# Kernel tuning notes

Measured on AMD Instinct MI355X. Metric: run time of the kernel, lower is better.

Reference implementation:

```python
import jax, jax.numpy as jnp
import numpy as np

EPS = 1e-07
GAMMA = 2.0
LAMBDA_DISCO = 1000.0


def _binary_entropy(target, output):
    x = jnp.clip(output, EPS, 1.0 - EPS)
    return -target * jnp.log(x) - (1.0 - target) * jnp.log(1.0 - x)


def _focal_bce(target, output, y_class, y_pred_class):
    yc = y_class[:, 0]
    ypc = y_pred_class[:, 0]
    y_pred = output[:, 0]
    bce = _binary_entropy(target, y_pred)
    m = jnp.mean(ypc)
    s = jnp.std(ypc)  # population std, matches tf.math.reduce_std
    norm = jnp.clip((ypc - m) / (2.0 * s) + 0.5, 0.0, 1.0)
    class_weight_factor = ((1.0 - yc) * norm) ** GAMMA
    norm_factor = jnp.sum(1.0 - yc) / jnp.sum(class_weight_factor)
    return class_weight_factor * bce * norm_factor


def _distance_corr(var_1, var_2, w, power):
    # pairwise |x_i - x_j| distance matrices [N, N]
    amat = jnp.abs(var_1[:, None] - var_1[None, :])
    bmat = jnp.abs(var_2[:, None] - var_2[None, :])
    amatavg = jnp.mean(amat * w, axis=1)
    bmatavg = jnp.mean(bmat * w, axis=1)
    # double centering (tile layout: minuend_1[i,j]=avg[j], minuend_2[i,j]=avg[i])
    Amat = amat - amatavg[None, :] - amatavg[:, None] + jnp.mean(amatavg * w)
    Bmat = bmat - bmatavg[None, :] - bmatavg[:, None] + jnp.mean(bmatavg * w)
    ABavg = jnp.abs(jnp.mean(Amat * Bmat * w, axis=1))
    AAavg = jnp.mean(Amat * Amat * w, axis=1)
    BBavg = jnp.mean(Bmat * Bmat * w, axis=1)
    mAB = jnp.mean(ABavg * w)
    mAA = jnp.mean(AAavg * w)
    mBB = jnp.mean(BBavg * w)
    if power == 1:
        dCorr = mAB / jnp.sqrt(jnp.abs(mAA * mBB) + 1e-12)
    elif power == 2:
        dCorr = mAB ** 2 / (jnp.abs(mAA * mBB) + 1e-12)
    else:
        dCorr = (mAB / jnp.sqrt(mAA * mBB) + 1e-12) ** power
    dCorr = jnp.where(jnp.isnan(dCorr), 0.0, dCorr)
    dCorr = jnp.where(dCorr < 0.0, 0.0, dCorr)
    return dCorr


def setup_inputs() -> dict:
    N = 4096
    key = jax.random.key(0)
    ks = jax.random.split(key, 6)
    target = jnp.round(jax.random.uniform(ks[0], (N,), dtype=jnp.float32))
    output = jax.random.uniform(ks[1], (N, 1), dtype=jnp.float32, minval=0.02, maxval=0.98)
    y_class = jnp.round(jax.random.uniform(ks[2], (N, 1), dtype=jnp.float32))
    y_pred_class = jax.random.uniform(ks[3], (N, 1), dtype=jnp.float32, minval=0.02, maxval=0.98)
    var_1 = jax.random.normal(ks[4], (N,), dtype=jnp.float32) * 20.0 + 100.0  # mass-like
    var_2 = jax.random.uniform(ks[5], (N,), dtype=jnp.float32)  # classifier-output-like
    normedweight = jnp.ones((N,), dtype=jnp.float32)  # sums to N as required
    return {"target": target, "output": output, "y_class": y_class,
            "y_pred_class": y_pred_class, "var_1": var_1, "var_2": var_2,
            "normedweight": normedweight, "power": 1}


def reference(target, output, y_class, y_pred_class, var_1, var_2, normedweight, power):
    focal = _focal_bce(target, output, y_class, y_pred_class)
    dcorr = _distance_corr(var_1, var_2, normedweight, power)
    return jnp.mean(focal) + LAMBDA_DISCO * dcorr
```

## Files before the change

### kernel.cpp

```cpp
#include <hip/hip_runtime.h>
#include <math.h>

#define N     4096
#define NBLK  256
#define RPB   16
#define FEPS  1e-7f


__device__ __forceinline__ double block_reduce(double v) {
    __shared__ double buf[4];
    int tid = threadIdx.x;
#pragma unroll
    for (int o = 32; o > 0; o >>= 1) v += __shfl_down(v, o, 64);
    __syncthreads();
    if ((tid & 63) == 0) buf[tid >> 6] = v;
    __syncthreads();
    return buf[0] + buf[1] + buf[2] + buf[3];
}

__global__ __launch_bounds__(256) void k1(
        const float* __restrict__ y_class,
        const float* __restrict__ y_pred_class,
        const float* __restrict__ v1,
        const float* __restrict__ v2,
        const float* __restrict__ w,
        double* __restrict__ pf,
        double* __restrict__ pg,
        float*  __restrict__ rowA,
        float*  __restrict__ rowB)
{
    __shared__ float s1[N], s2[N], sw[N];
    __shared__ float rsA[RPB], rsB[RPB];
    const int tid = threadIdx.x;
    const int b   = blockIdx.x;

    for (int t = tid * 4; t < N; t += 1024) {
        *(float4*)&s1[t] = *(const float4*)&v1[t];
        *(float4*)&s2[t] = *(const float4*)&v2[t];
        *(float4*)&sw[t] = *(const float4*)&w [t];
    }

    if (tid < 16) {
        int i = b * RPB + tid;
        float ypc = y_pred_class[i];
        float yc  = y_class[i];
        double sy  = (double)ypc;
        double sy2 = (double)ypc * (double)ypc;
        double syc = (double)yc;
#pragma unroll
        for (int o = 1; o < 16; o <<= 1) {
            sy  += __shfl_xor(sy,  o, 16);
            sy2 += __shfl_xor(sy2, o, 16);
            syc += __shfl_xor(syc, o, 16);
        }
        if (tid == 0) { pf[b] = sy; pf[NBLK + b] = sy2; pf[2 * NBLK + b] = syc; }
    }
    __syncthreads();

    const int lane = tid & 63;
    const int g    = tid >> 6;
    const int i0   = b * RPB + g * 4;
    float a0 = s1[i0+0], a1 = s1[i0+1], a2 = s1[i0+2], a3 = s1[i0+3];
    float e0 = s2[i0+0], e1 = s2[i0+1], e2 = s2[i0+2], e3 = s2[i0+3];
    float sa0=0.f,sa1=0.f,sa2=0.f,sa3=0.f, sb0=0.f,sb1=0.f,sb2=0.f,sb3=0.f;
#pragma unroll 4
    for (int k = 0; k < N / (64 * 4); ++k) {
        int j = 4 * lane + 256 * k;
        float4 x1 = *(const float4*)&s1[j];
        float4 x2 = *(const float4*)&s2[j];
        float4 xw = *(const float4*)&sw[j];
#define P1(c)                                      \
        sa0 = fmaf(fabsf(a0 - x1.c), xw.c, sa0);   \
        sa1 = fmaf(fabsf(a1 - x1.c), xw.c, sa1);   \
        sa2 = fmaf(fabsf(a2 - x1.c), xw.c, sa2);   \
        sa3 = fmaf(fabsf(a3 - x1.c), xw.c, sa3);   \
        sb0 = fmaf(fabsf(e0 - x2.c), xw.c, sb0);   \
        sb1 = fmaf(fabsf(e1 - x2.c), xw.c, sb1);   \
        sb2 = fmaf(fabsf(e2 - x2.c), xw.c, sb2);   \
        sb3 = fmaf(fabsf(e3 - x2.c), xw.c, sb3);
        P1(x) P1(y) P1(z) P1(w)
#undef P1
    }
#pragma unroll
    for (int o = 1; o < 64; o <<= 1) {
        sa0 += __shfl_xor(sa0, o, 64); sa1 += __shfl_xor(sa1, o, 64);
        sa2 += __shfl_xor(sa2, o, 64); sa3 += __shfl_xor(sa3, o, 64);
        sb0 += __shfl_xor(sb0, o, 64); sb1 += __shfl_xor(sb1, o, 64);
        sb2 += __shfl_xor(sb2, o, 64); sb3 += __shfl_xor(sb3, o, 64);
    }
    if (lane == 0) {
        rowA[i0+0]=sa0; rowA[i0+1]=sa1; rowA[i0+2]=sa2; rowA[i0+3]=sa3;
        rowB[i0+0]=sb0; rowB[i0+1]=sb1; rowB[i0+2]=sb2; rowB[i0+3]=sb3;
        rsA[g*4+0]=sa0; rsA[g*4+1]=sa1; rsA[g*4+2]=sa2; rsA[g*4+3]=sa3;
        rsB[g*4+0]=sb0; rsB[g*4+1]=sb1; rsB[g*4+2]=sb2; rsB[g*4+3]=sb3;
    }
    __syncthreads();
    if (tid == 0) {
        double ga = 0.0, gb = 0.0;
#pragma unroll
        for (int q = 0; q < RPB; ++q) {
            double wq = (double)sw[b * RPB + q];
            ga += (double)rsA[q] * wq;
            gb += (double)rsB[q] * wq;
        }
        pg[b] = ga; pg[NBLK + b] = gb;
    }
}

__global__ __launch_bounds__(256) void k2(
        const float* __restrict__ target,
        const float* __restrict__ output,
        const float* __restrict__ y_class,
        const float* __restrict__ y_pred_class,
        const float* __restrict__ v1,
        const float* __restrict__ v2,
        const float* __restrict__ w,
        const float* __restrict__ rowA,
        const float* __restrict__ rowB,
        const double* __restrict__ pf,
        const double* __restrict__ pg,
        const int*   __restrict__ power,
        unsigned int* __restrict__ cntB,
        double* __restrict__ pr,
        float*  __restrict__ out)
{
    __shared__ float s1[N], s2[N], sw[N], sav[N], sbv[N];
    __shared__ double rd[3][RPB];
    const int tid = threadIdx.x;
    const int b   = blockIdx.x;
    const float invN = 1.0f / (float)N;

    for (int t = tid * 4; t < N; t += 1024) {
        *(float4*)&s1[t] = *(const float4*)&v1[t];
        *(float4*)&s2[t] = *(const float4*)&v2[t];
        *(float4*)&sw[t] = *(const float4*)&w [t];
        float4 ra = *(const float4*)&rowA[t];
        float4 rb = *(const float4*)&rowB[t];
        ra.x *= invN; ra.y *= invN; ra.z *= invN; ra.w *= invN;
        rb.x *= invN; rb.y *= invN; rb.z *= invN; rb.w *= invN;
        *(float4*)&sav[t] = ra;
        *(float4*)&sbv[t] = rb;
    }
    __syncthreads();

    const double NN = (double)N * (double)N;
    float gA = (float)(block_reduce(pg[tid]) / NN);
    float gB = (float)(block_reduce(pg[NBLK + tid]) / NN);
    double t_ypc  = block_reduce(pf[tid]);
    double t_ypc2 = block_reduce(pf[NBLK + tid]);
    double fm   = t_ypc / (double)N;
    double fvar = t_ypc2 / (double)N - fm * fm;
    double fsd  = sqrt(fvar > 0.0 ? fvar : 0.0);
    float  m    = (float)fm;
    float  inv2s = (float)(1.0 / (2.0 * fsd));

    if (tid < 16) {
        int i = b * RPB + tid;
        float yc  = y_class[i];
        float ypc = y_pred_class[i];
        float nrm = (ypc - m) * inv2s + 0.5f;
        nrm = fminf(fmaxf(nrm, 0.0f), 1.0f);
        float c1  = (1.0f - yc) * nrm;
        float cwf = c1 * c1;
        float x = fminf(fmaxf(output[i], FEPS), 1.0f - FEPS);
        float t = target[i];
        float bce = -t * logf(x) - (1.0f - t) * logf(1.0f - x);
        double scwf  = (double)cwf;
        double scwfb = (double)cwf * (double)bce;
#pragma unroll
        for (int o = 1; o < 16; o <<= 1) {
            scwf  += __shfl_xor(scwf,  o, 16);
            scwfb += __shfl_xor(scwfb, o, 16);
        }
        if (tid == 0) { pr[3 * NBLK + b] = scwf; pr[4 * NBLK + b] = scwfb; }
    }

    const int lane = tid & 63;
    const int g    = tid >> 6;
    const int i0   = b * RPB + g * 4;
    float a0 = s1[i0+0], a1 = s1[i0+1], a2 = s1[i0+2], a3 = s1[i0+3];
    float e0 = s2[i0+0], e1 = s2[i0+1], e2 = s2[i0+2], e3 = s2[i0+3];
    float cA0 = sav[i0+0] - gA, cA1 = sav[i0+1] - gA,
          cA2 = sav[i0+2] - gA, cA3 = sav[i0+3] - gA;
    float cB0 = sbv[i0+0] - gB, cB1 = sbv[i0+1] - gB,
          cB2 = sbv[i0+2] - gB, cB3 = sbv[i0+3] - gB;

    float ab0=0.f,ab1=0.f,ab2=0.f,ab3=0.f;
    float aa0=0.f,aa1=0.f,aa2=0.f,aa3=0.f;
    float bb0=0.f,bb1=0.f,bb2=0.f,bb3=0.f;
#pragma unroll 2
    for (int k = 0; k < N / (64 * 4); ++k) {
        int j = 4 * lane + 256 * k;
        float4 x1 = *(const float4*)&s1[j];
        float4 x2 = *(const float4*)&s2[j];
        float4 xw = *(const float4*)&sw[j];
        float4 xa = *(const float4*)&sav[j];
        float4 xb = *(const float4*)&sbv[j];
#define P2(c, r)                                                  \
        {                                                         \
            float Am = fabsf(a##r - x1.c) - xa.c - cA##r;         \
            float Bm = fabsf(e##r - x2.c) - xb.c - cB##r;         \
            float Aw = Am * xw.c;                                 \
            float Bw = Bm * xw.c;                                 \
            ab##r = fmaf(Aw, Bm, ab##r);                          \
            aa##r = fmaf(Aw, Am, aa##r);                          \
            bb##r = fmaf(Bw, Bm, bb##r);                          \
        }
#define P2ALL(c) P2(c,0) P2(c,1) P2(c,2) P2(c,3)
        P2ALL(x) P2ALL(y) P2ALL(z) P2ALL(w)
#undef P2ALL
#undef P2
    }
#pragma unroll
    for (int o = 1; o < 64; o <<= 1) {
        ab0 += __shfl_xor(ab0, o, 64); ab1 += __shfl_xor(ab1, o, 64);
        ab2 += __shfl_xor(ab2, o, 64); ab3 += __shfl_xor(ab3, o, 64);
        aa0 += __shfl_xor(aa0, o, 64); aa1 += __shfl_xor(aa1, o, 64);
        aa2 += __shfl_xor(aa2, o, 64); aa3 += __shfl_xor(aa3, o, 64);
        bb0 += __shfl_xor(bb0, o, 64); bb1 += __shfl_xor(bb1, o, 64);
        bb2 += __shfl_xor(bb2, o, 64); bb3 += __shfl_xor(bb3, o, 64);
    }
    if (lane == 0) {
        double w0 = (double)sw[i0+0], w1 = (double)sw[i0+1];
        double w2 = (double)sw[i0+2], w3 = (double)sw[i0+3];
        rd[0][g*4+0] = fabs((double)ab0) * w0; rd[0][g*4+1] = fabs((double)ab1) * w1;
        rd[0][g*4+2] = fabs((double)ab2) * w2; rd[0][g*4+3] = fabs((double)ab3) * w3;
        rd[1][g*4+0] = (double)aa0 * w0;       rd[1][g*4+1] = (double)aa1 * w1;
        rd[1][g*4+2] = (double)aa2 * w2;       rd[1][g*4+3] = (double)aa3 * w3;
        rd[2][g*4+0] = (double)bb0 * w0;       rd[2][g*4+1] = (double)bb1 * w1;
        rd[2][g*4+2] = (double)bb2 * w2;       rd[2][g*4+3] = (double)bb3 * w3;
    }
    __syncthreads();

    __shared__ int isLast;
    if (tid == 0) {
        double tab = 0.0, taa = 0.0, tbb = 0.0;
#pragma unroll
        for (int q = 0; q < RPB; ++q) { tab += rd[0][q]; taa += rd[1][q]; tbb += rd[2][q]; }
        pr[b] = tab; pr[NBLK + b] = taa; pr[2 * NBLK + b] = tbb;
        __threadfence();
        unsigned int old = atomicAdd(cntB, 1u);
        isLast = (old == NBLK - 1);
    }
    __syncthreads();
    if (!isLast) return;
    __threadfence();

    double tab   = block_reduce(pr[tid]);
    double taa   = block_reduce(pr[NBLK + tid]);
    double tbb   = block_reduce(pr[2 * NBLK + tid]);
    double tcwf  = block_reduce(pr[3 * NBLK + tid]);
    double tcwfb = block_reduce(pr[4 * NBLK + tid]);
    double t_yc  = block_reduce(pf[2 * NBLK + tid]);
    if (tid == 0) {
        double focal = tcwfb * (((double)N - t_yc) / tcwf) / (double)N;
        double mAB = tab / NN;
        double mAA = taa / NN;
        double mBB = tbb / NN;
        int p = power[0];
        double d;
        if (p == 1) {
            d = mAB / sqrt(fabs(mAA * mBB) + 1e-12);
        } else if (p == 2) {
            d = (mAB * mAB) / (fabs(mAA * mBB) + 1e-12);
        } else {
            d = pow(mAB / sqrt(mAA * mBB) + 1e-12, (double)p);
        }
        if (isnan(d)) d = 0.0;
        if (d < 0.0)  d = 0.0;
        out[0] = (float)(focal + 1000.0 * d);
    }
}

extern "C" void kernel_launch(void* const* d_in, const int* in_sizes, int n_in,
                              void* d_out, int out_size, void* d_ws, size_t ws_size,
                              hipStream_t stream) {
    const float* target       = (const float*)d_in[0];
    const float* output       = (const float*)d_in[1];
    const float* y_class      = (const float*)d_in[2];
    const float* y_pred_class = (const float*)d_in[3];
    const float* var_1        = (const float*)d_in[4];
    const float* var_2        = (const float*)d_in[5];
    const float* normedweight = (const float*)d_in[6];
    const int*   power        = (const int*)d_in[7];
    float* out = (float*)d_out;

    char*         ws   = (char*)d_ws;
    unsigned int* cntB = (unsigned int*)ws;
    double*       pf   = (double*)(ws + 64);
    double*       pg   = (double*)(ws + 64 + 6144);
    double*       pr   = (double*)(ws + 64 + 6144 + 4096);
    float*        rowA = (float*)(ws + 64 + 6144 + 4096 + 10240);
    float*        rowB = rowA + N;

    hipMemsetAsync(ws, 0, 4, stream);
    k1<<<NBLK, 256, 0, stream>>>(y_class, y_pred_class, var_1, var_2, normedweight,
                                 pf, pg, rowA, rowB);
    k2<<<NBLK, 256, 0, stream>>>(target, output, y_class, y_pred_class,
                                 var_1, var_2, normedweight, rowA, rowB,
                                 pf, pg, power, cntB, pr, out);
}
```

Before: 36.48 us.

## Split work across 512 blocks with half-column tiles and drop memset launch

Raises the grid from 256 to 512 blocks. In k1 each block now covers one half of the columns and writes partial row sums per half. In k2 each block handles 8 rows and loops over two half-size shared tiles, so shared memory per block is halved and occupancy should rise. The counter reset moves from a separate hipMemsetAsync into k1, which removes one launch. In exchange k2 stages its shared data twice, with extra syncs and extra global reads of the partial rows.

```diff
diff --git a/kernel.cpp b/kernel.cpp
--- a/kernel.cpp
+++ b/kernel.cpp
@@ -2,8 +2,8 @@
 #include <math.h>
 
 #define N     4096
-#define NBLK  256
-#define RPB   16
+#define HALF  2048
+#define NB    512
 #define FEPS  1e-7f
 
 
@@ -24,24 +24,30 @@
         const float* __restrict__ v1,
         const float* __restrict__ v2,
         const float* __restrict__ w,
+        unsigned int* __restrict__ cntB,
         double* __restrict__ pf,
         double* __restrict__ pg,
-        float*  __restrict__ rowA,
-        float*  __restrict__ rowB)
+        float*  __restrict__ rowA_p,
+        float*  __restrict__ rowB_p)
 {
-    __shared__ float s1[N], s2[N], sw[N];
-    __shared__ float rsA[RPB], rsB[RPB];
+    __shared__ float s1[HALF], s2[HALF], sw[HALF];
+    __shared__ float rsA[16], rsB[16];
     const int tid = threadIdx.x;
     const int b   = blockIdx.x;
-
-    for (int t = tid * 4; t < N; t += 1024) {
-        *(float4*)&s1[t] = *(const float4*)&v1[t];
-        *(float4*)&s2[t] = *(const float4*)&v2[t];
-        *(float4*)&sw[t] = *(const float4*)&w [t];
-    }
-
-    if (tid < 16) {
-        int i = b * RPB + tid;
+    const int rb  = b >> 1;
+    const int h   = b & 1;
+    const int j0  = h * HALF;
+
+    if (b == 0 && tid == 0) *cntB = 0;
+
+    for (int t = tid * 4; t < HALF; t += 1024) {
+        *(float4*)&s1[t] = *(const float4*)&v1[j0 + t];
+        *(float4*)&s2[t] = *(const float4*)&v2[j0 + t];
+        *(float4*)&sw[t] = *(const float4*)&w [j0 + t];
+    }
+
+    if (h == 0 && tid < 16) {
+        int i = rb * 16 + tid;
         float ypc = y_pred_class[i];
         float yc  = y_class[i];
         double sy  = (double)ypc;
@@ -53,18 +59,18 @@
             sy2 += __shfl_xor(sy2, o, 16);
             syc += __shfl_xor(syc, o, 16);
         }
-        if (tid == 0) { pf[b] = sy; pf[NBLK + b] = sy2; pf[2 * NBLK + b] = syc; }
+        if (tid == 0) { pf[rb] = sy; pf[256 + rb] = sy2; pf[512 + rb] = syc; }
     }
     __syncthreads();
 
     const int lane = tid & 63;
     const int g    = tid >> 6;
-    const int i0   = b * RPB + g * 4;
-    float a0 = s1[i0+0], a1 = s1[i0+1], a2 = s1[i0+2], a3 = s1[i0+3];
-    float e0 = s2[i0+0], e1 = s2[i0+1], e2 = s2[i0+2], e3 = s2[i0+3];
+    const int i0   = rb * 16 + g * 4;
+    float a0 = v1[i0+0], a1 = v1[i0+1], a2 = v1[i0+2], a3 = v1[i0+3];
+    float e0 = v2[i0+0], e1 = v2[i0+1], e2 = v2[i0+2], e3 = v2[i0+3];
     float sa0=0.f,sa1=0.f,sa2=0.f,sa3=0.f, sb0=0.f,sb1=0.f,sb2=0.f,sb3=0.f;
-#pragma unroll 4
-    for (int k = 0; k < N / (64 * 4); ++k) {
+#pragma unroll
+    for (int k = 0; k < HALF / (64 * 4); ++k) {
         int j = 4 * lane + 256 * k;
         float4 x1 = *(const float4*)&s1[j];
         float4 x2 = *(const float4*)&s2[j];
@@ -89,21 +95,24 @@
         sb2 += __shfl_xor(sb2, o, 64); sb3 += __shfl_xor(sb3, o, 64);
     }
     if (lane == 0) {
-        rowA[i0+0]=sa0; rowA[i0+1]=sa1; rowA[i0+2]=sa2; rowA[i0+3]=sa3;
-        rowB[i0+0]=sb0; rowB[i0+1]=sb1; rowB[i0+2]=sb2; rowB[i0+3]=sb3;
+        rowA_p[h*N + i0+0]=sa0; rowA_p[h*N + i0+1]=sa1;
+        rowA_p[h*N + i0+2]=sa2; rowA_p[h*N + i0+3]=sa3;
+        rowB_p[h*N + i0+0]=sb0; rowB_p[h*N + i0+1]=sb1;
+        rowB_p[h*N + i0+2]=sb2; rowB_p[h*N + i0+3]=sb3;
         rsA[g*4+0]=sa0; rsA[g*4+1]=sa1; rsA[g*4+2]=sa2; rsA[g*4+3]=sa3;
         rsB[g*4+0]=sb0; rsB[g*4+1]=sb1; rsB[g*4+2]=sb2; rsB[g*4+3]=sb3;
     }
     __syncthreads();
-    if (tid == 0) {
-        double ga = 0.0, gb = 0.0;
-#pragma unroll
-        for (int q = 0; q < RPB; ++q) {
-            double wq = (double)sw[b * RPB + q];
-            ga += (double)rsA[q] * wq;
-            gb += (double)rsB[q] * wq;
-        }
-        pg[b] = ga; pg[NBLK + b] = gb;
+    if (tid < 16) {
+        double wq = (double)w[rb * 16 + tid];
+        double da = (double)rsA[tid] * wq;
+        double db = (double)rsB[tid] * wq;
+#pragma unroll
+        for (int o = 1; o < 16; o <<= 1) {
+            da += __shfl_xor(da, o, 16);
+            db += __shfl_xor(db, o, 16);
+        }
+        if (tid == 0) { pg[b] = da; pg[NB + b] = db; }
     }
 }
 
@@ -115,8 +124,8 @@
         const float* __restrict__ v1,
         const float* __restrict__ v2,
         const float* __restrict__ w,
-        const float* __restrict__ rowA,
-        const float* __restrict__ rowB,
+        const float* __restrict__ rowA_p,
+        const float* __restrict__ rowB_p,
         const double* __restrict__ pf,
         const double* __restrict__ pg,
         const int*   __restrict__ power,
@@ -124,38 +133,25 @@
         double* __restrict__ pr,
         float*  __restrict__ out)
 {
-    __shared__ float s1[N], s2[N], sw[N], sav[N], sbv[N];
-    __shared__ double rd[3][RPB];
+    __shared__ float s1[HALF], s2[HALF], sw[HALF], sav[HALF], sbv[HALF];
+    __shared__ double rd[3][8];
     const int tid = threadIdx.x;
     const int b   = blockIdx.x;
     const float invN = 1.0f / (float)N;
-
-    for (int t = tid * 4; t < N; t += 1024) {
-        *(float4*)&s1[t] = *(const float4*)&v1[t];
-        *(float4*)&s2[t] = *(const float4*)&v2[t];
-        *(float4*)&sw[t] = *(const float4*)&w [t];
-        float4 ra = *(const float4*)&rowA[t];
-        float4 rb = *(const float4*)&rowB[t];
-        ra.x *= invN; ra.y *= invN; ra.z *= invN; ra.w *= invN;
-        rb.x *= invN; rb.y *= invN; rb.z *= invN; rb.w *= invN;
-        *(float4*)&sav[t] = ra;
-        *(float4*)&sbv[t] = rb;
-    }
-    __syncthreads();
-
     const double NN = (double)N * (double)N;
-    float gA = (float)(block_reduce(pg[tid]) / NN);
-    float gB = (float)(block_reduce(pg[NBLK + tid]) / NN);
+
+    float gA = (float)(block_reduce(pg[tid]      + pg[256 + tid]) / NN);
+    float gB = (float)(block_reduce(pg[NB + tid] + pg[NB + 256 + tid]) / NN);
     double t_ypc  = block_reduce(pf[tid]);
-    double t_ypc2 = block_reduce(pf[NBLK + tid]);
+    double t_ypc2 = block_reduce(pf[256 + tid]);
     double fm   = t_ypc / (double)N;
     double fvar = t_ypc2 / (double)N - fm * fm;
     double fsd  = sqrt(fvar > 0.0 ? fvar : 0.0);
-    float  m    = (float)fm;
+    float  m     = (float)fm;
     float  inv2s = (float)(1.0 / (2.0 * fsd));
 
-    if (tid < 16) {
-        int i = b * RPB + tid;
+    if (b < 256 && tid < 16) {
+        int i = b * 16 + tid;
         float yc  = y_class[i];
         float ypc = y_pred_class[i];
         float nrm = (ypc - m) * inv2s + 0.5f;
@@ -172,63 +168,75 @@
             scwf  += __shfl_xor(scwf,  o, 16);
             scwfb += __shfl_xor(scwfb, o, 16);
         }
-        if (tid == 0) { pr[3 * NBLK + b] = scwf; pr[4 * NBLK + b] = scwfb; }
+        if (tid == 0) { pr[3 * NB + b] = scwf; pr[3 * NB + 256 + b] = scwfb; }
     }
 
     const int lane = tid & 63;
     const int g    = tid >> 6;
-    const int i0   = b * RPB + g * 4;
-    float a0 = s1[i0+0], a1 = s1[i0+1], a2 = s1[i0+2], a3 = s1[i0+3];
-    float e0 = s2[i0+0], e1 = s2[i0+1], e2 = s2[i0+2], e3 = s2[i0+3];
-    float cA0 = sav[i0+0] - gA, cA1 = sav[i0+1] - gA,
-          cA2 = sav[i0+2] - gA, cA3 = sav[i0+3] - gA;
-    float cB0 = sbv[i0+0] - gB, cB1 = sbv[i0+1] - gB,
-          cB2 = sbv[i0+2] - gB, cB3 = sbv[i0+3] - gB;
-
-    float ab0=0.f,ab1=0.f,ab2=0.f,ab3=0.f;
-    float aa0=0.f,aa1=0.f,aa2=0.f,aa3=0.f;
-    float bb0=0.f,bb1=0.f,bb2=0.f,bb3=0.f;
-#pragma unroll 2
-    for (int k = 0; k < N / (64 * 4); ++k) {
-        int j = 4 * lane + 256 * k;
-        float4 x1 = *(const float4*)&s1[j];
-        float4 x2 = *(const float4*)&s2[j];
-        float4 xw = *(const float4*)&sw[j];
-        float4 xa = *(const float4*)&sav[j];
-        float4 xb = *(const float4*)&sbv[j];
+    const int i0   = b * 8 + g * 2;
+    float a0 = v1[i0+0], a1 = v1[i0+1];
+    float e0 = v2[i0+0], e1 = v2[i0+1];
+    float cA0 = (rowA_p[i0+0] + rowA_p[N+i0+0]) * invN - gA;
+    float cA1 = (rowA_p[i0+1] + rowA_p[N+i0+1]) * invN - gA;
+    float cB0 = (rowB_p[i0+0] + rowB_p[N+i0+0]) * invN - gB;
+    float cB1 = (rowB_p[i0+1] + rowB_p[N+i0+1]) * invN - gB;
+
+    float ab0=0.f,aa0=0.f,bb0=0.f, ab1=0.f,aa1=0.f,bb1=0.f;
+    for (int h = 0; h < 2; ++h) {
+        int j0 = h * HALF;
+        __syncthreads();
+        for (int t = tid * 4; t < HALF; t += 1024) {
+            *(float4*)&s1[t] = *(const float4*)&v1[j0 + t];
+            *(float4*)&s2[t] = *(const float4*)&v2[j0 + t];
+            *(float4*)&sw[t] = *(const float4*)&w [j0 + t];
+            float4 r0 = *(const float4*)&rowA_p[j0 + t];
+            float4 r1 = *(const float4*)&rowA_p[N + j0 + t];
+            float4 q0 = *(const float4*)&rowB_p[j0 + t];
+            float4 q1 = *(const float4*)&rowB_p[N + j0 + t];
+            float4 ra, rbv;
+            ra.x  = (r0.x + r1.x) * invN;  ra.y  = (r0.y + r1.y) * invN;
+            ra.z  = (r0.z + r1.z) * invN;  ra.w  = (r0.w + r1.w) * invN;
+            rbv.x = (q0.x + q1.x) * invN;  rbv.y = (q0.y + q1.y) * invN;
+            rbv.z = (q0.z + q1.z) * invN;  rbv.w = (q0.w + q1.w) * invN;
+            *(float4*)&sav[t] = ra;
+            *(float4*)&sbv[t] = rbv;
+        }
+        __syncthreads();
+#pragma unroll
+        for (int k = 0; k < HALF / (64 * 4); ++k) {
+            int j = 4 * lane + 256 * k;
+            float4 x1 = *(const float4*)&s1[j];
+            float4 x2 = *(const float4*)&s2[j];
+            float4 xw = *(const float4*)&sw[j];
+            float4 xa = *(const float4*)&sav[j];
+            float4 xb = *(const float4*)&sbv[j];
 #define P2(c, r)                                                  \
-        {                                                         \
-            float Am = fabsf(a##r - x1.c) - xa.c - cA##r;         \
-            float Bm = fabsf(e##r - x2.c) - xb.c - cB##r;         \
-            float Aw = Am * xw.c;                                 \
-            float Bw = Bm * xw.c;                                 \
-            ab##r = fmaf(Aw, Bm, ab##r);                          \
-            aa##r = fmaf(Aw, Am, aa##r);                          \
-            bb##r = fmaf(Bw, Bm, bb##r);                          \
-        }
-#define P2ALL(c) P2(c,0) P2(c,1) P2(c,2) P2(c,3)
-        P2ALL(x) P2ALL(y) P2ALL(z) P2ALL(w)
+            {                                                     \
+                float Am = fabsf(a##r - x1.c) - xa.c - cA##r;     \
+                float Bm = fabsf(e##r - x2.c) - xb.c - cB##r;     \
+                float Aw = Am * xw.c;                             \
+                float Bw = Bm * xw.c;                             \
+                ab##r = fmaf(Aw, Bm, ab##r);                      \
+                aa##r = fmaf(Aw, Am, aa##r);                      \
+                bb##r = fmaf(Bw, Bm, bb##r);                      \
+            }
+#define P2ALL(c) P2(c,0) P2(c,1)
+            P2ALL(x) P2ALL(y) P2ALL(z) P2ALL(w)
 #undef P2ALL
 #undef P2
+        }
     }
 #pragma unroll
     for (int o = 1; o < 64; o <<= 1) {
         ab0 += __shfl_xor(ab0, o, 64); ab1 += __shfl_xor(ab1, o, 64);
-        ab2 += __shfl_xor(ab2, o, 64); ab3 += __shfl_xor(ab3, o, 64);
         aa0 += __shfl_xor(aa0, o, 64); aa1 += __shfl_xor(aa1, o, 64);
-        aa2 += __shfl_xor(aa2, o, 64); aa3 += __shfl_xor(aa3, o, 64);
         bb0 += __shfl_xor(bb0, o, 64); bb1 += __shfl_xor(bb1, o, 64);
-        bb2 += __shfl_xor(bb2, o, 64); bb3 += __shfl_xor(bb3, o, 64);
     }
     if (lane == 0) {
-        double w0 = (double)sw[i0+0], w1 = (double)sw[i0+1];
-        double w2 = (double)sw[i0+2], w3 = (double)sw[i0+3];
-        rd[0][g*4+0] = fabs((double)ab0) * w0; rd[0][g*4+1] = fabs((double)ab1) * w1;
-        rd[0][g*4+2] = fabs((double)ab2) * w2; rd[0][g*4+3] = fabs((double)ab3) * w3;
-        rd[1][g*4+0] = (double)aa0 * w0;       rd[1][g*4+1] = (double)aa1 * w1;
-        rd[1][g*4+2] = (double)aa2 * w2;       rd[1][g*4+3] = (double)aa3 * w3;
-        rd[2][g*4+0] = (double)bb0 * w0;       rd[2][g*4+1] = (double)bb1 * w1;
-        rd[2][g*4+2] = (double)bb2 * w2;       rd[2][g*4+3] = (double)bb3 * w3;
+        double w0 = (double)w[i0+0], w1 = (double)w[i0+1];
+        rd[0][g*2+0] = fabs((double)ab0) * w0;  rd[0][g*2+1] = fabs((double)ab1) * w1;
+        rd[1][g*2+0] = (double)aa0 * w0;        rd[1][g*2+1] = (double)aa1 * w1;
+        rd[2][g*2+0] = (double)bb0 * w0;        rd[2][g*2+1] = (double)bb1 * w1;
     }
     __syncthreads();
 
@@ -236,22 +244,22 @@
     if (tid == 0) {
         double tab = 0.0, taa = 0.0, tbb = 0.0;
 #pragma unroll
-        for (int q = 0; q < RPB; ++q) { tab += rd[0][q]; taa += rd[1][q]; tbb += rd[2][q]; }
-        pr[b] = tab; pr[NBLK + b] = taa; pr[2 * NBLK + b] = tbb;
+        for (int q = 0; q < 8; ++q) { tab += rd[0][q]; taa += rd[1][q]; tbb += rd[2][q]; }
+        pr[b] = tab; pr[NB + b] = taa; pr[2 * NB + b] = tbb;
         __threadfence();
         unsigned int old = atomicAdd(cntB, 1u);
-        isLast = (old == NBLK - 1);
+        isLast = (old == NB - 1);
     }
     __syncthreads();
     if (!isLast) return;
     __threadfence();
 
-    double tab   = block_reduce(pr[tid]);
-    double taa   = block_reduce(pr[NBLK + tid]);
-    double tbb   = block_reduce(pr[2 * NBLK + tid]);
-    double tcwf  = block_reduce(pr[3 * NBLK + tid]);
-    double tcwfb = block_reduce(pr[4 * NBLK + tid]);
-    double t_yc  = block_reduce(pf[2 * NBLK + tid]);
+    double tab   = block_reduce(pr[tid]          + pr[256 + tid]);
+    double taa   = block_reduce(pr[NB + tid]     + pr[NB + 256 + tid]);
+    double tbb   = block_reduce(pr[2*NB + tid]   + pr[2*NB + 256 + tid]);
+    double tcwf  = block_reduce(pr[3*NB + tid]);
+    double tcwfb = block_reduce(pr[3*NB + 256 + tid]);
+    double t_yc  = block_reduce(pf[512 + tid]);
     if (tid == 0) {
         double focal = tcwfb * (((double)N - t_yc) / tcwf) / (double)N;
         double mAB = tab / NN;
@@ -285,18 +293,17 @@
     const int*   power        = (const int*)d_in[7];
     float* out = (float*)d_out;
 
-    char*         ws   = (char*)d_ws;
-    unsigned int* cntB = (unsigned int*)ws;
-    double*       pf   = (double*)(ws + 64);
-    double*       pg   = (double*)(ws + 64 + 6144);
-    double*       pr   = (double*)(ws + 64 + 6144 + 4096);
-    float*        rowA = (float*)(ws + 64 + 6144 + 4096 + 10240);
-    float*        rowB = rowA + N;
-
-    hipMemsetAsync(ws, 0, 4, stream);
-    k1<<<NBLK, 256, 0, stream>>>(y_class, y_pred_class, var_1, var_2, normedweight,
-                                 pf, pg, rowA, rowB);
-    k2<<<NBLK, 256, 0, stream>>>(target, output, y_class, y_pred_class,
-                                 var_1, var_2, normedweight, rowA, rowB,
-                                 pf, pg, power, cntB, pr, out);
+    char*         ws     = (char*)d_ws;
+    unsigned int* cntB   = (unsigned int*)ws;
+    double*       pf     = (double*)(ws + 64);
+    double*       pg     = (double*)(ws + 64 + 6144);
+    double*       pr     = (double*)(ws + 64 + 6144 + 8192);
+    float*        rowA_p = (float*)(ws + 64 + 6144 + 8192 + 16384);
+    float*        rowB_p = rowA_p + 2 * N;
+
+    k1<<<NB, 256, 0, stream>>>(y_class, y_pred_class, var_1, var_2, normedweight,
+                               cntB, pf, pg, rowA_p, rowB_p);
+    k2<<<NB, 256, 0, stream>>>(target, output, y_class, y_pred_class,
+                               var_1, var_2, normedweight, rowA_p, rowB_p,
+                               pf, pg, power, cntB, pr, out);
 }
```

After: 35.00 us. -4.1%, faster.
